# Kernel optimization log

Hardware: AMD Instinct MI355X
Metric: run time of the kernel (lower is better)

Reference implementation:

```python
import jax, jax.numpy as jnp
import numpy as np

COST_CLASS = 1.0
COST_COORD = 1.0
ALPHA = 0.25
GAMMA = 2.0
EPS = 1e-8
B, N = 4, 512


def setup_inputs() -> dict:
    key = jax.random.key(0)
    k1, k2, k3 = jax.random.split(key, 3)
    return {
        "pred_logits": jax.random.normal(k1, (B, N), dtype=jnp.float32),
        "pred_points": jax.random.uniform(k2, (B, N, 2), dtype=jnp.float32),
        "gt_points": jax.random.uniform(k3, (B, N, 2), dtype=jnp.float32),
        "gt_mask": jnp.ones((B, N), dtype=bool),
    }


def _cost_matrix(pred_logits, pred_points, gt_points):
    # focal-style classification cost, depends only on the prediction -> column-constant
    prob = jax.nn.sigmoid(pred_logits)                       # [B, N]
    neg = (1.0 - ALPHA) * prob ** GAMMA * (-jnp.log(1.0 - prob + EPS))
    pos = ALPHA * (1.0 - prob) ** GAMMA * (-jnp.log(prob + EPS))
    cost_class = (pos - neg)[:, :, None]                     # [B, N, 1]
    # L1 cdist between pred_points and gt_points
    cost_coord = jnp.sum(
        jnp.abs(pred_points[:, :, None, :] - gt_points[:, None, :, :]), axis=-1
    )                                                        # [B, N, N]
    return COST_CLASS * cost_class + COST_COORD * cost_coord


def _lsa(cost):
    # Jonker-Volgenant shortest augmenting path (e-maxx Hungarian), square, minimization.
    c = np.asarray(cost, dtype=np.float64)
    n = c.shape[0]
    INF = 1e18
    u = np.zeros(n + 1)
    v = np.zeros(n + 1)
    p = np.zeros(n + 1, dtype=np.int64)   # p[j] = row matched to column j (1-based)
    way = np.zeros(n + 1, dtype=np.int64)
    for i in range(1, n + 1):
        p[0] = i
        j0 = 0
        minv = np.full(n + 1, INF)
        used = np.zeros(n + 1, dtype=bool)
        while True:
            used[j0] = True
            i0 = p[j0]
            cur = c[i0 - 1] - u[i0] - v[1:]
            nu = ~used[1:]
            mv = minv[1:]
            wy = way[1:]
            upd = nu & (cur < mv)
            mv[upd] = cur[upd]
            wy[upd] = j0
            cand = np.where(nu, mv, INF)
            j1 = int(np.argmin(cand)) + 1
            delta = cand[j1 - 1]
            u[p[used]] += delta
            v[used] -= delta
            mv[nu] -= delta
            j0 = j1
            if p[j0] == 0:
                break
        while j0:
            j1 = int(way[j0])
            p[j0] = int(p[j1])
            j0 = j1
    col_of_row = np.empty(n, dtype=np.int64)
    col_of_row[p[1:] - 1] = np.arange(n)
    return np.arange(n), col_of_row


def reference(pred_logits, pred_points, gt_points, gt_mask):
    C = _cost_matrix(pred_logits, pred_points, gt_points)   # [B, N, N]
    mask = np.asarray(gt_mask)
    assert mask.all(), "reference assumes all gt slots valid (static shapes)"
    Cn = np.asarray(jax.device_get(C))
    pred_idx, gt_idx = [], []
    for b in range(Cn.shape[0]):
        r, c = _lsa(Cn[b])
        pred_idx.append(r)
        gt_idx.append(c)
    pred_idx = jnp.asarray(np.stack(pred_idx))
    gt_idx = jnp.asarray(np.stack(gt_idx))
    return pred_idx, gt_idx, C
```

## Files before the change

### kernel.cpp

```cpp
#include <hip/hip_runtime.h>
#include <math.h>

constexpr int B_ = 4;
constexpr int N_ = 512;

__device__ __forceinline__ float cephes_expf(float xin) {
#pragma clang fp contract(off)
    float x = fminf(xin, 88.3762626647950f);
    x = fmaxf(x, -88.3762626647949f);
    float fx = x * 1.44269504088896341f;
    fx = fx + 0.5f;
    fx = floorf(fx);
    float tmp = fx * 0.693359375f;
    float z0  = fx * -2.12194440e-4f;
    float r = x - tmp;
    r = r - z0;
    float zz = r * r;
    float y = 1.9875691500E-4f;
    y = y * r + 1.3981999507E-3f;
    y = y * r + 8.3334519073E-3f;
    y = y * r + 4.1665795894E-2f;
    y = y * r + 1.6666665459E-1f;
    y = y * r + 5.0000001201E-1f;
    y = y * zz + r;
    y = y + 1.0f;
    int n = (int)fx;
    float p2n = __uint_as_float((unsigned)(n + 0x7f) << 23);
    float res = y * p2n;
    return fmaxf(res, xin);
}

__device__ __forceinline__ float cephes_logf(float t) {
#pragma clang fp contract(off)
    float xx = fmaxf(t, 1.17549435e-38f);
    unsigned u = __float_as_uint(xx);
    int e_i = (int)(u >> 23) - 0x7f;
    float e = (float)e_i + 1.0f;
    float m = __uint_as_float((u & 0x807fffffu) | 0x3f000000u);
    int mask = (m < 0.707106781186547524f);
    float tmp1 = mask ? m : 0.0f;
    float x = m - 1.0f;
    e = e - (mask ? 1.0f : 0.0f);
    x = x + tmp1;
    float z = x * x;
    float y = 7.0376836292E-2f;
    y = y * x + -1.1514610310E-1f;
    y = y * x + 1.1676998740E-1f;
    y = y * x + -1.2420140846E-1f;
    y = y * x + 1.4249322787E-1f;
    y = y * x + -1.6668057665E-1f;
    y = y * x + 2.0000714765E-1f;
    y = y * x + -2.4999993993E-1f;
    y = y * x + 3.3333331174E-1f;
    y = y * x;
    y = y * z;
    y = e * -2.12194440e-4f + y;
    y = y - z * 0.5f;
    float res = x + y;
    res = res + e * 0.693359375f;
    return res;
}

__global__ __launch_bounds__(256) void class_cost_kernel(
    const float* __restrict__ logits, float* __restrict__ cc_out)
{
#pragma clang fp contract(off)
    int idx = blockIdx.x * 256 + threadIdx.x;
    if (idx >= B_ * N_) return;
    float x    = logits[idx];
    float e    = cephes_expf(-x);
    float prob = 1.0f / (1.0f + e);
    float om   = 1.0f - prob;
    float p2   = prob * prob;
    float o2   = om * om;
    float lneg = cephes_logf(om   + 1e-8f);
    float lpos = cephes_logf(prob + 1e-8f);
    float neg  = (0.75f * p2) * (-lneg);
    float pos  = (0.25f * o2) * (-lpos);
    cc_out[idx] = pos - neg;
}

__global__ __launch_bounds__(512) void cost_kernel(
    const float* __restrict__ cc,
    const float* __restrict__ pred_pts,
    const float* __restrict__ gt_pts,
    float* __restrict__ C)
{
    int blk = blockIdx.x;
    int b = blk >> 9;
    int i = blk & (N_ - 1);
    int j = threadIdx.x;

    const float2* pp2 = reinterpret_cast<const float2*>(pred_pts);
    const float2* gp2 = reinterpret_cast<const float2*>(gt_pts);
    float2 pp = pp2[b * N_ + i];
    float2 gp = gp2[b * N_ + j];
    float coord = fabsf(pp.x - gp.x) + fabsf(pp.y - gp.y);

    C[(size_t)b * N_ * N_ + (size_t)i * N_ + j] = cc[blk] + coord;
}

template<int CTRL>
__device__ __forceinline__ uint32_t dpp32(uint32_t x) {
    return (uint32_t)__builtin_amdgcn_update_dpp((int)x, (int)x, CTRL, 0xF, 0xF, false);
}
#define UMINSTEP(X, CTRL) { uint32_t o_ = dpp32<CTRL>(X); X = (o_ < X) ? o_ : X; }

__device__ __forceinline__ uint32_t wave_umin_lane63(uint32_t x) {
    UMINSTEP(x, 0x111) UMINSTEP(x, 0x112) UMINSTEP(x, 0x114)
    UMINSTEP(x, 0x118) UMINSTEP(x, 0x142) UMINSTEP(x, 0x143)
    return x;
}

__device__ __forceinline__ double readlane_f64(double d, int lane) {
    unsigned long long ll = (unsigned long long)__double_as_longlong(d);
    unsigned lo = (unsigned)__builtin_amdgcn_readlane((int)(unsigned)ll, lane);
    unsigned hi = (unsigned)__builtin_amdgcn_readlane((int)(unsigned)(ll >> 32), lane);
    return __longlong_as_double((long long)(((unsigned long long)hi << 32) | lo));
}

__global__ __launch_bounds__(64, 1) void solve_kernel(
    const float* __restrict__ cc_in,
    const float* __restrict__ pred_pts,
    const float* __restrict__ gt_pts,
    float* __restrict__ pred_idx,
    float* __restrict__ gt_idx)
{
    const int b = blockIdx.x;
    const int t = threadIdx.x;

    const float2* pq = reinterpret_cast<const float2*>(pred_pts) + b * N_;
    const float2* gq = reinterpret_cast<const float2*>(gt_pts)   + b * N_;
    const float*  cq = cc_in + b * N_;
    const int base = t << 3;

    float2 r0 = pq[base + 0], r1 = pq[base + 1], r2 = pq[base + 2], r3 = pq[base + 3];
    float2 r4 = pq[base + 4], r5 = pq[base + 5], r6 = pq[base + 6], r7 = pq[base + 7];
    float2 g0 = gq[base + 0], g1 = gq[base + 1], g2 = gq[base + 2], g3 = gq[base + 3];
    float2 g4 = gq[base + 4], g5 = gq[base + 5], g6 = gq[base + 6], g7 = gq[base + 7];
    float  c0 = cq[base + 0], c1 = cq[base + 1], c2 = cq[base + 2], c3 = cq[base + 3];
    float  c4 = cq[base + 4], c5 = cq[base + 5], c6 = cq[base + 6], c7 = cq[base + 7];

    double u0=0.0,u1=0.0,u2=0.0,u3=0.0,u4=0.0,u5=0.0,u6=0.0,u7=0.0;
    double v0=0.0,v1=0.0,v2=0.0,v3=0.0,v4=0.0,v5=0.0,v6=0.0,v7=0.0;
    int    p0=-1,p1=-1,p2=-1,p3=-1,p4=-1,p5=-1,p6=-1,p7=-1;

    #pragma unroll
    for (int k = 0; k < 8; ++k)
        pred_idx[b * N_ + t + 64 * k] = (float)(t + 64 * k);

    #define SEL8F(sl, x0,x1,x2,x3,x4,x5,x6,x7, out) {                      \
        float a0_=((sl)&1)?(x1):(x0), a1_=((sl)&1)?(x3):(x2);              \
        float a2_=((sl)&1)?(x5):(x4), a3_=((sl)&1)?(x7):(x6);              \
        float b0_=((sl)&2)?a1_:a0_,   b1_=((sl)&2)?a3_:a2_;                \
        out = ((sl)&4)?b1_:b0_; }
    #define SEL8I(sl, x0,x1,x2,x3,x4,x5,x6,x7, out) {                      \
        int a0_=((sl)&1)?(x1):(x0), a1_=((sl)&1)?(x3):(x2);                \
        int a2_=((sl)&1)?(x5):(x4), a3_=((sl)&1)?(x7):(x6);                \
        int b0_=((sl)&2)?a1_:a0_,   b1_=((sl)&2)?a3_:a2_;                  \
        out = ((sl)&4)?b1_:b0_; }
    #define SEL8D(sl, x0,x1,x2,x3,x4,x5,x6,x7, out) {                      \
        double a0_=((sl)&1)?(x1):(x0), a1_=((sl)&1)?(x3):(x2);             \
        double a2_=((sl)&1)?(x5):(x4), a3_=((sl)&1)?(x7):(x6);             \
        double b0_=((sl)&2)?a1_:a0_,   b1_=((sl)&2)?a3_:a2_;               \
        out = ((sl)&4)?b1_:b0_; }

    float px_r, py_r, cc_r; double urow;
    #define ROW_SCALARS(r) {                                               \
        int sl_ = (r) & 7, ln_ = (r) >> 3;                                 \
        float sx_, sy_, sc_; double su_;                                   \
        SEL8F(sl_, r0.x,r1.x,r2.x,r3.x,r4.x,r5.x,r6.x,r7.x, sx_);          \
        SEL8F(sl_, r0.y,r1.y,r2.y,r3.y,r4.y,r5.y,r6.y,r7.y, sy_);          \
        SEL8F(sl_, c0,c1,c2,c3,c4,c5,c6,c7, sc_);                          \
        SEL8D(sl_, u0,u1,u2,u3,u4,u5,u6,u7, su_);                          \
        px_r = __uint_as_float((unsigned)__builtin_amdgcn_readlane(        \
                   (int)__float_as_uint(sx_), ln_));                       \
        py_r = __uint_as_float((unsigned)__builtin_amdgcn_readlane(        \
                   (int)__float_as_uint(sy_), ln_));                       \
        cc_r = __uint_as_float((unsigned)__builtin_amdgcn_readlane(        \
                   (int)__float_as_uint(sc_), ln_));                       \
        urow = readlane_f64(su_, ln_); }

    const float INF32 = __uint_as_float(0x7F800000u);

    for (int i = 0; i < N_; ++i) {
        unsigned used_m  = 0u;
        unsigned chain_m = (t == (i >> 3)) ? (1u << (i & 7)) : 0u;
        ROW_SCALARS(i);

        for (;;) {
#pragma clang fp contract(off)
            float w0 = cc_r + (fabsf(px_r - g0.x) + fabsf(py_r - g0.y));
            float w1 = cc_r + (fabsf(px_r - g1.x) + fabsf(py_r - g1.y));
            float w2 = cc_r + (fabsf(px_r - g2.x) + fabsf(py_r - g2.y));
            float w3 = cc_r + (fabsf(px_r - g3.x) + fabsf(py_r - g3.y));
            float w4 = cc_r + (fabsf(px_r - g4.x) + fabsf(py_r - g4.y));
            float w5 = cc_r + (fabsf(px_r - g5.x) + fabsf(py_r - g5.y));
            float w6 = cc_r + (fabsf(px_r - g6.x) + fabsf(py_r - g6.y));
            float w7 = cc_r + (fabsf(px_r - g7.x) + fabsf(py_r - g7.y));
            w0 = (used_m & 0x01u) ? INF32 : w0;
            w1 = (used_m & 0x02u) ? INF32 : w1;
            w2 = (used_m & 0x04u) ? INF32 : w2;
            w3 = (used_m & 0x08u) ? INF32 : w3;
            w4 = (used_m & 0x10u) ? INF32 : w4;
            w5 = (used_m & 0x20u) ? INF32 : w5;
            w6 = (used_m & 0x40u) ? INF32 : w6;
            w7 = (used_m & 0x80u) ? INF32 : w7;

            double d0 = ((double)w0 - urow) - v0;
            double d1 = ((double)w1 - urow) - v1;
            double d2 = ((double)w2 - urow) - v2;
            double d3 = ((double)w3 - urow) - v3;
            double d4 = ((double)w4 - urow) - v4;
            double d5 = ((double)w5 - urow) - v5;
            double d6 = ((double)w6 - urow) - v6;
            double d7 = ((double)w7 - urow) - v7;

            double  ka = (d1 < d0) ? d1 : d0;  uint32_t sa = (d1 < d0) ? 1u : 0u;
            double  kb = (d3 < d2) ? d3 : d2;  uint32_t sb = (d3 < d2) ? 3u : 2u;
            double  kx = (d5 < d4) ? d5 : d4;  uint32_t sx = (d5 < d4) ? 5u : 4u;
            double  kd = (d7 < d6) ? d7 : d6;  uint32_t sd = (d7 < d6) ? 7u : 6u;
            double  ke = (kb < ka) ? kb : ka;  uint32_t se = (kb < ka) ? sb : sa;
            double  kf = (kd < kx) ? kd : kx;  uint32_t sf = (kd < kx) ? sd : sx;
            double  bv = (kf < ke) ? kf : ke;  uint32_t bslot = (kf < ke) ? sf : se;

            uint64_t kb64 = (uint64_t)__double_as_longlong(bv);
            kb64 ^= (kb64 >> 63) ? 0xFFFFFFFFFFFFFFFFull : 0x8000000000000000ull;
            uint32_t khi = (uint32_t)(kb64 >> 32);
            uint32_t klo = (uint32_t)kb64;

            int own_pre;
            SEL8I(bslot, p0,p1,p2,p3,p4,p5,p6,p7, own_pre);

            uint32_t Mhi = (uint32_t)__builtin_amdgcn_readlane(
                               (int)wave_umin_lane63(khi), 63);
            unsigned long long tied_hi = __ballot(khi == Mhi);

            int lane1; uint32_t Mlo;
            if (__builtin_popcountll(tied_hi) == 1) {
                lane1 = (int)__builtin_ctzll(tied_hi);
                Mlo = (uint32_t)__builtin_amdgcn_readlane((int)klo, lane1);
            } else {
                uint32_t kl2 = (khi == Mhi) ? klo : 0xFFFFFFFFu;
                Mlo = (uint32_t)__builtin_amdgcn_readlane(
                          (int)wave_umin_lane63(kl2), 63);
                lane1 = (int)__builtin_ctzll(__ballot(khi == Mhi && klo == Mlo));
            }

            int slot1 = __builtin_amdgcn_readlane((int)bslot, lane1);
            int owner = __builtin_amdgcn_readlane(own_pre, lane1);

            uint64_t M = ((uint64_t)Mhi << 32) | Mlo;
            uint64_t db = (M >> 63) ? (M ^ 0x8000000000000000ull) : ~M;
            double delta = __longlong_as_double((long long)db);

            if (owner < 0) {
                u0 += (chain_m & 0x01u) ? delta : 0.0;
                u1 += (chain_m & 0x02u) ? delta : 0.0;
                u2 += (chain_m & 0x04u) ? delta : 0.0;
                u3 += (chain_m & 0x08u) ? delta : 0.0;
                u4 += (chain_m & 0x10u) ? delta : 0.0;
                u5 += (chain_m & 0x20u) ? delta : 0.0;
                u6 += (chain_m & 0x40u) ? delta : 0.0;
                u7 += (chain_m & 0x80u) ? delta : 0.0;
                v0 -= (used_m  & 0x01u) ? delta : 0.0;
                v1 -= (used_m  & 0x02u) ? delta : 0.0;
                v2 -= (used_m  & 0x04u) ? delta : 0.0;
                v3 -= (used_m  & 0x08u) ? delta : 0.0;
                v4 -= (used_m  & 0x10u) ? delta : 0.0;
                v5 -= (used_m  & 0x20u) ? delta : 0.0;
                v6 -= (used_m  & 0x40u) ? delta : 0.0;
                v7 -= (used_m  & 0x80u) ? delta : 0.0;
                bool mine = (t == lane1);
                p0 = (mine && slot1 == 0) ? i : p0;
                p1 = (mine && slot1 == 1) ? i : p1;
                p2 = (mine && slot1 == 2) ? i : p2;
                p3 = (mine && slot1 == 3) ? i : p3;
                p4 = (mine && slot1 == 4) ? i : p4;
                p5 = (mine && slot1 == 5) ? i : p5;
                p6 = (mine && slot1 == 6) ? i : p6;
                p7 = (mine && slot1 == 7) ? i : p7;
                break;
            }

            ROW_SCALARS(owner);

            u0 += (chain_m & 0x01u) ? delta : 0.0;
            u1 += (chain_m & 0x02u) ? delta : 0.0;
            u2 += (chain_m & 0x04u) ? delta : 0.0;
            u3 += (chain_m & 0x08u) ? delta : 0.0;
            u4 += (chain_m & 0x10u) ? delta : 0.0;
            u5 += (chain_m & 0x20u) ? delta : 0.0;
            u6 += (chain_m & 0x40u) ? delta : 0.0;
            u7 += (chain_m & 0x80u) ? delta : 0.0;
            v0 -= (used_m  & 0x01u) ? delta : 0.0;
            v1 -= (used_m  & 0x02u) ? delta : 0.0;
            v2 -= (used_m  & 0x04u) ? delta : 0.0;
            v3 -= (used_m  & 0x08u) ? delta : 0.0;
            v4 -= (used_m  & 0x10u) ? delta : 0.0;
            v5 -= (used_m  & 0x20u) ? delta : 0.0;
            v6 -= (used_m  & 0x40u) ? delta : 0.0;
            v7 -= (used_m  & 0x80u) ? delta : 0.0;

            used_m  |= (t == lane1)        ? (1u << slot1)       : 0u;
            chain_m |= (t == (owner >> 3)) ? (1u << (owner & 7)) : 0u;
        }
    }

    gt_idx[b * N_ + p0] = (float)(base);
    gt_idx[b * N_ + p1] = (float)(base + 1);
    gt_idx[b * N_ + p2] = (float)(base + 2);
    gt_idx[b * N_ + p3] = (float)(base + 3);
    gt_idx[b * N_ + p4] = (float)(base + 4);
    gt_idx[b * N_ + p5] = (float)(base + 5);
    gt_idx[b * N_ + p6] = (float)(base + 6);
    gt_idx[b * N_ + p7] = (float)(base + 7);
}

extern "C" void kernel_launch(void* const* d_in, const int* in_sizes, int n_in,
                              void* d_out, int out_size, void* d_ws, size_t ws_size,
                              hipStream_t stream)
{
    const float* logits   = (const float*)d_in[0];
    const float* pred_pts = (const float*)d_in[1];
    const float* gt_pts   = (const float*)d_in[2];

    float* out      = (float*)d_out;
    float* pred_idx = out;
    float* gt_idx   = out + B_ * N_;
    float* C        = out + 2 * B_ * N_;
    float* cc       = (float*)d_ws;

    class_cost_kernel<<<(B_ * N_ + 255) / 256, 256, 0, stream>>>(logits, cc);
    cost_kernel<<<B_ * N_, N_, 0, stream>>>(cc, pred_pts, gt_pts, C);
    solve_kernel<<<B_, 64, 0, stream>>>(cc, pred_pts, gt_pts, pred_idx, gt_idx);
}
```

Before: 1.646 ms.

## Interleave two batch Hungarian solves per wave to hide serial latency

Each wavefront now solves two batch items at once, alternating one augmenting step of each inside a single flat loop so their independent dependency chains can overlap. The nested row/augment loops become a branch-free state machine that handles the terminal step with selects and prefetches the next row's scalars unconditionally. The single-tie fast path for the cross-lane argmin is dropped, so the second min reduction always runs. The trade-offs are that each step now covers two problems, more registers are used per lane, and only two waves are launched, so wall time follows the longer of each pair of solves.

```diff
diff --git a/kernel.cpp b/kernel.cpp
--- a/kernel.cpp
+++ b/kernel.cpp
@@ -119,6 +119,149 @@
     return __longlong_as_double((long long)(((unsigned long long)hi << 32) | lo));
 }
 
+#define SEL8F(sl, x0,x1,x2,x3,x4,x5,x6,x7, out) {                      \
+    float a0_=((sl)&1)?(x1):(x0), a1_=((sl)&1)?(x3):(x2);              \
+    float a2_=((sl)&1)?(x5):(x4), a3_=((sl)&1)?(x7):(x6);              \
+    float b0_=((sl)&2)?a1_:a0_,   b1_=((sl)&2)?a3_:a2_;                \
+    out = ((sl)&4)?b1_:b0_; }
+#define SEL8I(sl, x0,x1,x2,x3,x4,x5,x6,x7, out) {                      \
+    int a0_=((sl)&1)?(x1):(x0), a1_=((sl)&1)?(x3):(x2);                \
+    int a2_=((sl)&1)?(x5):(x4), a3_=((sl)&1)?(x7):(x6);                \
+    int b0_=((sl)&2)?a1_:a0_,   b1_=((sl)&2)?a3_:a2_;                  \
+    out = ((sl)&4)?b1_:b0_; }
+#define SEL8D(sl, x0,x1,x2,x3,x4,x5,x6,x7, out) {                      \
+    double a0_=((sl)&1)?(x1):(x0), a1_=((sl)&1)?(x3):(x2);             \
+    double a2_=((sl)&1)?(x5):(x4), a3_=((sl)&1)?(x7):(x6);             \
+    double b0_=((sl)&2)?a1_:a0_,   b1_=((sl)&2)?a3_:a2_;               \
+    out = ((sl)&4)?b1_:b0_; }
+
+#define DECL_LOAD(S, b)                                                       \
+    const float2* pq##S = reinterpret_cast<const float2*>(pred_pts) + (b) * N_; \
+    const float2* gq##S = reinterpret_cast<const float2*>(gt_pts)   + (b) * N_; \
+    const float*  cq##S = cc_in + (b) * N_;                                   \
+    float2 r0##S = pq##S[base+0], r1##S = pq##S[base+1];                      \
+    float2 r2##S = pq##S[base+2], r3##S = pq##S[base+3];                      \
+    float2 r4##S = pq##S[base+4], r5##S = pq##S[base+5];                      \
+    float2 r6##S = pq##S[base+6], r7##S = pq##S[base+7];                      \
+    float2 g0##S = gq##S[base+0], g1##S = gq##S[base+1];                      \
+    float2 g2##S = gq##S[base+2], g3##S = gq##S[base+3];                      \
+    float2 g4##S = gq##S[base+4], g5##S = gq##S[base+5];                      \
+    float2 g6##S = gq##S[base+6], g7##S = gq##S[base+7];                      \
+    float  c0##S = cq##S[base+0], c1##S = cq##S[base+1];                      \
+    float  c2##S = cq##S[base+2], c3##S = cq##S[base+3];                      \
+    float  c4##S = cq##S[base+4], c5##S = cq##S[base+5];                      \
+    float  c6##S = cq##S[base+6], c7##S = cq##S[base+7];                      \
+    double u0##S=0.0,u1##S=0.0,u2##S=0.0,u3##S=0.0;                           \
+    double u4##S=0.0,u5##S=0.0,u6##S=0.0,u7##S=0.0;                           \
+    double v0##S=0.0,v1##S=0.0,v2##S=0.0,v3##S=0.0;                           \
+    double v4##S=0.0,v5##S=0.0,v6##S=0.0,v7##S=0.0;                           \
+    int    p0##S=-1,p1##S=-1,p2##S=-1,p3##S=-1;                               \
+    int    p4##S=-1,p5##S=-1,p6##S=-1,p7##S=-1;                               \
+    unsigned used_m##S = 0u;                                                  \
+    unsigned chain_m##S = (t == 0) ? 1u : 0u;                                 \
+    int i##S = 0;                                                             \
+    float px_r##S, py_r##S, cc_r##S; double urow##S;
+
+#define ROW_SCALARS_S(S, r) {                                                 \
+    int sl_ = (r) & 7, ln_ = (r) >> 3;                                        \
+    float sx_, sy_, sc_; double su_;                                          \
+    SEL8F(sl_, r0##S.x,r1##S.x,r2##S.x,r3##S.x,r4##S.x,r5##S.x,r6##S.x,r7##S.x, sx_); \
+    SEL8F(sl_, r0##S.y,r1##S.y,r2##S.y,r3##S.y,r4##S.y,r5##S.y,r6##S.y,r7##S.y, sy_); \
+    SEL8F(sl_, c0##S,c1##S,c2##S,c3##S,c4##S,c5##S,c6##S,c7##S, sc_);         \
+    SEL8D(sl_, u0##S,u1##S,u2##S,u3##S,u4##S,u5##S,u6##S,u7##S, su_);         \
+    px_r##S = __uint_as_float((unsigned)__builtin_amdgcn_readlane(            \
+                  (int)__float_as_uint(sx_), ln_));                           \
+    py_r##S = __uint_as_float((unsigned)__builtin_amdgcn_readlane(            \
+                  (int)__float_as_uint(sy_), ln_));                           \
+    cc_r##S = __uint_as_float((unsigned)__builtin_amdgcn_readlane(            \
+                  (int)__float_as_uint(sc_), ln_));                           \
+    urow##S = readlane_f64(su_, ln_); }
+
+#define STEP(S) {                                                             \
+    float w0 = cc_r##S + (fabsf(px_r##S - g0##S.x) + fabsf(py_r##S - g0##S.y)); \
+    float w1 = cc_r##S + (fabsf(px_r##S - g1##S.x) + fabsf(py_r##S - g1##S.y)); \
+    float w2 = cc_r##S + (fabsf(px_r##S - g2##S.x) + fabsf(py_r##S - g2##S.y)); \
+    float w3 = cc_r##S + (fabsf(px_r##S - g3##S.x) + fabsf(py_r##S - g3##S.y)); \
+    float w4 = cc_r##S + (fabsf(px_r##S - g4##S.x) + fabsf(py_r##S - g4##S.y)); \
+    float w5 = cc_r##S + (fabsf(px_r##S - g5##S.x) + fabsf(py_r##S - g5##S.y)); \
+    float w6 = cc_r##S + (fabsf(px_r##S - g6##S.x) + fabsf(py_r##S - g6##S.y)); \
+    float w7 = cc_r##S + (fabsf(px_r##S - g7##S.x) + fabsf(py_r##S - g7##S.y)); \
+    w0 = (used_m##S & 0x01u) ? INF32 : w0;                                    \
+    w1 = (used_m##S & 0x02u) ? INF32 : w1;                                    \
+    w2 = (used_m##S & 0x04u) ? INF32 : w2;                                    \
+    w3 = (used_m##S & 0x08u) ? INF32 : w3;                                    \
+    w4 = (used_m##S & 0x10u) ? INF32 : w4;                                    \
+    w5 = (used_m##S & 0x20u) ? INF32 : w5;                                    \
+    w6 = (used_m##S & 0x40u) ? INF32 : w6;                                    \
+    w7 = (used_m##S & 0x80u) ? INF32 : w7;                                    \
+    double d0 = ((double)w0 - urow##S) - v0##S;                               \
+    double d1 = ((double)w1 - urow##S) - v1##S;                               \
+    double d2 = ((double)w2 - urow##S) - v2##S;                               \
+    double d3 = ((double)w3 - urow##S) - v3##S;                               \
+    double d4 = ((double)w4 - urow##S) - v4##S;                               \
+    double d5 = ((double)w5 - urow##S) - v5##S;                               \
+    double d6 = ((double)w6 - urow##S) - v6##S;                               \
+    double d7 = ((double)w7 - urow##S) - v7##S;                               \
+    double  ka = (d1 < d0) ? d1 : d0;  uint32_t sa = (d1 < d0) ? 1u : 0u;     \
+    double  kb = (d3 < d2) ? d3 : d2;  uint32_t sb = (d3 < d2) ? 3u : 2u;     \
+    double  kx = (d5 < d4) ? d5 : d4;  uint32_t sx = (d5 < d4) ? 5u : 4u;     \
+    double  kd = (d7 < d6) ? d7 : d6;  uint32_t sd = (d7 < d6) ? 7u : 6u;     \
+    double  ke = (kb < ka) ? kb : ka;  uint32_t se = (kb < ka) ? sb : sa;     \
+    double  kf = (kd < kx) ? kd : kx;  uint32_t sf = (kd < kx) ? sd : sx;     \
+    double  bv = (kf < ke) ? kf : ke;  uint32_t bslot = (kf < ke) ? sf : se;  \
+    uint64_t kb64 = (uint64_t)__double_as_longlong(bv);                       \
+    kb64 ^= (kb64 >> 63) ? 0xFFFFFFFFFFFFFFFFull : 0x8000000000000000ull;     \
+    uint32_t khi = (uint32_t)(kb64 >> 32);                                    \
+    uint32_t klo = (uint32_t)kb64;                                            \
+    int own_pre;                                                              \
+    SEL8I(bslot, p0##S,p1##S,p2##S,p3##S,p4##S,p5##S,p6##S,p7##S, own_pre);   \
+    uint32_t Mhi = (uint32_t)__builtin_amdgcn_readlane(                       \
+                       (int)wave_umin_lane63(khi), 63);                       \
+    uint32_t kl2 = (khi == Mhi) ? klo : 0xFFFFFFFFu;                          \
+    uint32_t Mlo = (uint32_t)__builtin_amdgcn_readlane(                       \
+                       (int)wave_umin_lane63(kl2), 63);                       \
+    int lane1 = (int)__builtin_ctzll(__ballot(khi == Mhi && klo == Mlo));     \
+    int slot1 = __builtin_amdgcn_readlane((int)bslot, lane1);                 \
+    int owner = __builtin_amdgcn_readlane(own_pre, lane1);                    \
+    uint64_t M = ((uint64_t)Mhi << 32) | Mlo;                                 \
+    uint64_t db = (M >> 63) ? (M ^ 0x8000000000000000ull) : ~M;               \
+    double delta = __longlong_as_double((long long)db);                       \
+    int terminal = (owner < 0) ? 1 : 0;                                       \
+    int nxt  = terminal ? (i##S + 1) : owner;                                 \
+    int nxtc = (nxt > (N_ - 1)) ? (N_ - 1) : nxt;                             \
+    ROW_SCALARS_S(S, nxtc);                                                   \
+    u0##S += (chain_m##S & 0x01u) ? delta : 0.0;                              \
+    u1##S += (chain_m##S & 0x02u) ? delta : 0.0;                              \
+    u2##S += (chain_m##S & 0x04u) ? delta : 0.0;                              \
+    u3##S += (chain_m##S & 0x08u) ? delta : 0.0;                              \
+    u4##S += (chain_m##S & 0x10u) ? delta : 0.0;                              \
+    u5##S += (chain_m##S & 0x20u) ? delta : 0.0;                              \
+    u6##S += (chain_m##S & 0x40u) ? delta : 0.0;                              \
+    u7##S += (chain_m##S & 0x80u) ? delta : 0.0;                              \
+    v0##S -= (used_m##S  & 0x01u) ? delta : 0.0;                              \
+    v1##S -= (used_m##S  & 0x02u) ? delta : 0.0;                              \
+    v2##S -= (used_m##S  & 0x04u) ? delta : 0.0;                              \
+    v3##S -= (used_m##S  & 0x08u) ? delta : 0.0;                              \
+    v4##S -= (used_m##S  & 0x10u) ? delta : 0.0;                              \
+    v5##S -= (used_m##S  & 0x20u) ? delta : 0.0;                              \
+    v6##S -= (used_m##S  & 0x40u) ? delta : 0.0;                              \
+    v7##S -= (used_m##S  & 0x80u) ? delta : 0.0;                              \
+    bool mine = (t == lane1);                                                 \
+    p0##S = (terminal && mine && slot1 == 0) ? i##S : p0##S;                  \
+    p1##S = (terminal && mine && slot1 == 1) ? i##S : p1##S;                  \
+    p2##S = (terminal && mine && slot1 == 2) ? i##S : p2##S;                  \
+    p3##S = (terminal && mine && slot1 == 3) ? i##S : p3##S;                  \
+    p4##S = (terminal && mine && slot1 == 4) ? i##S : p4##S;                  \
+    p5##S = (terminal && mine && slot1 == 5) ? i##S : p5##S;                  \
+    p6##S = (terminal && mine && slot1 == 6) ? i##S : p6##S;                  \
+    p7##S = (terminal && mine && slot1 == 7) ? i##S : p7##S;                  \
+    unsigned hopbit = (t == (nxt >> 3)) ? (1u << (nxt & 7)) : 0u;             \
+    unsigned selbit = mine ? (1u << slot1) : 0u;                              \
+    chain_m##S = terminal ? hopbit : (chain_m##S | hopbit);                   \
+    used_m##S  = terminal ? 0u     : (used_m##S  | selbit);                   \
+    i##S += terminal;                                                         \
+}
+
 __global__ __launch_bounds__(64, 1) void solve_kernel(
     const float* __restrict__ cc_in,
     const float* __restrict__ pred_pts,
@@ -126,195 +269,48 @@
     float* __restrict__ pred_idx,
     float* __restrict__ gt_idx)
 {
-    const int b = blockIdx.x;
-    const int t = threadIdx.x;
-
-    const float2* pq = reinterpret_cast<const float2*>(pred_pts) + b * N_;
-    const float2* gq = reinterpret_cast<const float2*>(gt_pts)   + b * N_;
-    const float*  cq = cc_in + b * N_;
+#pragma clang fp contract(off)
+    const int t  = threadIdx.x;
+    const int bA = blockIdx.x * 2;
+    const int bB = bA + 1;
     const int base = t << 3;
-
-    float2 r0 = pq[base + 0], r1 = pq[base + 1], r2 = pq[base + 2], r3 = pq[base + 3];
-    float2 r4 = pq[base + 4], r5 = pq[base + 5], r6 = pq[base + 6], r7 = pq[base + 7];
-    float2 g0 = gq[base + 0], g1 = gq[base + 1], g2 = gq[base + 2], g3 = gq[base + 3];
-    float2 g4 = gq[base + 4], g5 = gq[base + 5], g6 = gq[base + 6], g7 = gq[base + 7];
-    float  c0 = cq[base + 0], c1 = cq[base + 1], c2 = cq[base + 2], c3 = cq[base + 3];
-    float  c4 = cq[base + 4], c5 = cq[base + 5], c6 = cq[base + 6], c7 = cq[base + 7];
-
-    double u0=0.0,u1=0.0,u2=0.0,u3=0.0,u4=0.0,u5=0.0,u6=0.0,u7=0.0;
-    double v0=0.0,v1=0.0,v2=0.0,v3=0.0,v4=0.0,v5=0.0,v6=0.0,v7=0.0;
-    int    p0=-1,p1=-1,p2=-1,p3=-1,p4=-1,p5=-1,p6=-1,p7=-1;
+    const float INF32 = __uint_as_float(0x7F800000u);
+
+    DECL_LOAD(A, bA)
+    DECL_LOAD(B, bB)
 
     #pragma unroll
-    for (int k = 0; k < 8; ++k)
-        pred_idx[b * N_ + t + 64 * k] = (float)(t + 64 * k);
-
-    #define SEL8F(sl, x0,x1,x2,x3,x4,x5,x6,x7, out) {                      \
-        float a0_=((sl)&1)?(x1):(x0), a1_=((sl)&1)?(x3):(x2);              \
-        float a2_=((sl)&1)?(x5):(x4), a3_=((sl)&1)?(x7):(x6);              \
-        float b0_=((sl)&2)?a1_:a0_,   b1_=((sl)&2)?a3_:a2_;                \
-        out = ((sl)&4)?b1_:b0_; }
-    #define SEL8I(sl, x0,x1,x2,x3,x4,x5,x6,x7, out) {                      \
-        int a0_=((sl)&1)?(x1):(x0), a1_=((sl)&1)?(x3):(x2);                \
-        int a2_=((sl)&1)?(x5):(x4), a3_=((sl)&1)?(x7):(x6);                \
-        int b0_=((sl)&2)?a1_:a0_,   b1_=((sl)&2)?a3_:a2_;                  \
-        out = ((sl)&4)?b1_:b0_; }
-    #define SEL8D(sl, x0,x1,x2,x3,x4,x5,x6,x7, out) {                      \
-        double a0_=((sl)&1)?(x1):(x0), a1_=((sl)&1)?(x3):(x2);             \
-        double a2_=((sl)&1)?(x5):(x4), a3_=((sl)&1)?(x7):(x6);             \
-        double b0_=((sl)&2)?a1_:a0_,   b1_=((sl)&2)?a3_:a2_;               \
-        out = ((sl)&4)?b1_:b0_; }
-
-    float px_r, py_r, cc_r; double urow;
-    #define ROW_SCALARS(r) {                                               \
-        int sl_ = (r) & 7, ln_ = (r) >> 3;                                 \
-        float sx_, sy_, sc_; double su_;                                   \
-        SEL8F(sl_, r0.x,r1.x,r2.x,r3.x,r4.x,r5.x,r6.x,r7.x, sx_);          \
-        SEL8F(sl_, r0.y,r1.y,r2.y,r3.y,r4.y,r5.y,r6.y,r7.y, sy_);          \
-        SEL8F(sl_, c0,c1,c2,c3,c4,c5,c6,c7, sc_);                          \
-        SEL8D(sl_, u0,u1,u2,u3,u4,u5,u6,u7, su_);                          \
-        px_r = __uint_as_float((unsigned)__builtin_amdgcn_readlane(        \
-                   (int)__float_as_uint(sx_), ln_));                       \
-        py_r = __uint_as_float((unsigned)__builtin_amdgcn_readlane(        \
-                   (int)__float_as_uint(sy_), ln_));                       \
-        cc_r = __uint_as_float((unsigned)__builtin_amdgcn_readlane(        \
-                   (int)__float_as_uint(sc_), ln_));                       \
-        urow = readlane_f64(su_, ln_); }
-
-    const float INF32 = __uint_as_float(0x7F800000u);
-
-    for (int i = 0; i < N_; ++i) {
-        unsigned used_m  = 0u;
-        unsigned chain_m = (t == (i >> 3)) ? (1u << (i & 7)) : 0u;
-        ROW_SCALARS(i);
-
-        for (;;) {
-#pragma clang fp contract(off)
-            float w0 = cc_r + (fabsf(px_r - g0.x) + fabsf(py_r - g0.y));
-            float w1 = cc_r + (fabsf(px_r - g1.x) + fabsf(py_r - g1.y));
-            float w2 = cc_r + (fabsf(px_r - g2.x) + fabsf(py_r - g2.y));
-            float w3 = cc_r + (fabsf(px_r - g3.x) + fabsf(py_r - g3.y));
-            float w4 = cc_r + (fabsf(px_r - g4.x) + fabsf(py_r - g4.y));
-            float w5 = cc_r + (fabsf(px_r - g5.x) + fabsf(py_r - g5.y));
-            float w6 = cc_r + (fabsf(px_r - g6.x) + fabsf(py_r - g6.y));
-            float w7 = cc_r + (fabsf(px_r - g7.x) + fabsf(py_r - g7.y));
-            w0 = (used_m & 0x01u) ? INF32 : w0;
-            w1 = (used_m & 0x02u) ? INF32 : w1;
-            w2 = (used_m & 0x04u) ? INF32 : w2;
-            w3 = (used_m & 0x08u) ? INF32 : w3;
-            w4 = (used_m & 0x10u) ? INF32 : w4;
-            w5 = (used_m & 0x20u) ? INF32 : w5;
-            w6 = (used_m & 0x40u) ? INF32 : w6;
-            w7 = (used_m & 0x80u) ? INF32 : w7;
-
-            double d0 = ((double)w0 - urow) - v0;
-            double d1 = ((double)w1 - urow) - v1;
-            double d2 = ((double)w2 - urow) - v2;
-            double d3 = ((double)w3 - urow) - v3;
-            double d4 = ((double)w4 - urow) - v4;
-            double d5 = ((double)w5 - urow) - v5;
-            double d6 = ((double)w6 - urow) - v6;
-            double d7 = ((double)w7 - urow) - v7;
-
-            double  ka = (d1 < d0) ? d1 : d0;  uint32_t sa = (d1 < d0) ? 1u : 0u;
-            double  kb = (d3 < d2) ? d3 : d2;  uint32_t sb = (d3 < d2) ? 3u : 2u;
-            double  kx = (d5 < d4) ? d5 : d4;  uint32_t sx = (d5 < d4) ? 5u : 4u;
-            double  kd = (d7 < d6) ? d7 : d6;  uint32_t sd = (d7 < d6) ? 7u : 6u;
-            double  ke = (kb < ka) ? kb : ka;  uint32_t se = (kb < ka) ? sb : sa;
-            double  kf = (kd < kx) ? kd : kx;  uint32_t sf = (kd < kx) ? sd : sx;
-            double  bv = (kf < ke) ? kf : ke;  uint32_t bslot = (kf < ke) ? sf : se;
-
-            uint64_t kb64 = (uint64_t)__double_as_longlong(bv);
-            kb64 ^= (kb64 >> 63) ? 0xFFFFFFFFFFFFFFFFull : 0x8000000000000000ull;
-            uint32_t khi = (uint32_t)(kb64 >> 32);
-            uint32_t klo = (uint32_t)kb64;
-
-            int own_pre;
-            SEL8I(bslot, p0,p1,p2,p3,p4,p5,p6,p7, own_pre);
-
-            uint32_t Mhi = (uint32_t)__builtin_amdgcn_readlane(
-                               (int)wave_umin_lane63(khi), 63);
-            unsigned long long tied_hi = __ballot(khi == Mhi);
-
-            int lane1; uint32_t Mlo;
-            if (__builtin_popcountll(tied_hi) == 1) {
-                lane1 = (int)__builtin_ctzll(tied_hi);
-                Mlo = (uint32_t)__builtin_amdgcn_readlane((int)klo, lane1);
-            } else {
-                uint32_t kl2 = (khi == Mhi) ? klo : 0xFFFFFFFFu;
-                Mlo = (uint32_t)__builtin_amdgcn_readlane(
-                          (int)wave_umin_lane63(kl2), 63);
-                lane1 = (int)__builtin_ctzll(__ballot(khi == Mhi && klo == Mlo));
-            }
-
-            int slot1 = __builtin_amdgcn_readlane((int)bslot, lane1);
-            int owner = __builtin_amdgcn_readlane(own_pre, lane1);
-
-            uint64_t M = ((uint64_t)Mhi << 32) | Mlo;
-            uint64_t db = (M >> 63) ? (M ^ 0x8000000000000000ull) : ~M;
-            double delta = __longlong_as_double((long long)db);
-
-            if (owner < 0) {
-                u0 += (chain_m & 0x01u) ? delta : 0.0;
-                u1 += (chain_m & 0x02u) ? delta : 0.0;
-                u2 += (chain_m & 0x04u) ? delta : 0.0;
-                u3 += (chain_m & 0x08u) ? delta : 0.0;
-                u4 += (chain_m & 0x10u) ? delta : 0.0;
-                u5 += (chain_m & 0x20u) ? delta : 0.0;
-                u6 += (chain_m & 0x40u) ? delta : 0.0;
-                u7 += (chain_m & 0x80u) ? delta : 0.0;
-                v0 -= (used_m  & 0x01u) ? delta : 0.0;
-                v1 -= (used_m  & 0x02u) ? delta : 0.0;
-                v2 -= (used_m  & 0x04u) ? delta : 0.0;
-                v3 -= (used_m  & 0x08u) ? delta : 0.0;
-                v4 -= (used_m  & 0x10u) ? delta : 0.0;
-                v5 -= (used_m  & 0x20u) ? delta : 0.0;
-                v6 -= (used_m  & 0x40u) ? delta : 0.0;
-                v7 -= (used_m  & 0x80u) ? delta : 0.0;
-                bool mine = (t == lane1);
-                p0 = (mine && slot1 == 0) ? i : p0;
-                p1 = (mine && slot1 == 1) ? i : p1;
-                p2 = (mine && slot1 == 2) ? i : p2;
-                p3 = (mine && slot1 == 3) ? i : p3;
-                p4 = (mine && slot1 == 4) ? i : p4;
-                p5 = (mine && slot1 == 5) ? i : p5;
-                p6 = (mine && slot1 == 6) ? i : p6;
-                p7 = (mine && slot1 == 7) ? i : p7;
-                break;
-            }
-
-            ROW_SCALARS(owner);
-
-            u0 += (chain_m & 0x01u) ? delta : 0.0;
-            u1 += (chain_m & 0x02u) ? delta : 0.0;
-            u2 += (chain_m & 0x04u) ? delta : 0.0;
-            u3 += (chain_m & 0x08u) ? delta : 0.0;
-            u4 += (chain_m & 0x10u) ? delta : 0.0;
-            u5 += (chain_m & 0x20u) ? delta : 0.0;
-            u6 += (chain_m & 0x40u) ? delta : 0.0;
-            u7 += (chain_m & 0x80u) ? delta : 0.0;
-            v0 -= (used_m  & 0x01u) ? delta : 0.0;
-            v1 -= (used_m  & 0x02u) ? delta : 0.0;
-            v2 -= (used_m  & 0x04u) ? delta : 0.0;
-            v3 -= (used_m  & 0x08u) ? delta : 0.0;
-            v4 -= (used_m  & 0x10u) ? delta : 0.0;
-            v5 -= (used_m  & 0x20u) ? delta : 0.0;
-            v6 -= (used_m  & 0x40u) ? delta : 0.0;
-            v7 -= (used_m  & 0x80u) ? delta : 0.0;
-
-            used_m  |= (t == lane1)        ? (1u << slot1)       : 0u;
-            chain_m |= (t == (owner >> 3)) ? (1u << (owner & 7)) : 0u;
-        }
+    for (int k = 0; k < 8; ++k) {
+        pred_idx[bA * N_ + t + 64 * k] = (float)(t + 64 * k);
+        pred_idx[bB * N_ + t + 64 * k] = (float)(t + 64 * k);
     }
 
-    gt_idx[b * N_ + p0] = (float)(base);
-    gt_idx[b * N_ + p1] = (float)(base + 1);
-    gt_idx[b * N_ + p2] = (float)(base + 2);
-    gt_idx[b * N_ + p3] = (float)(base + 3);
-    gt_idx[b * N_ + p4] = (float)(base + 4);
-    gt_idx[b * N_ + p5] = (float)(base + 5);
-    gt_idx[b * N_ + p6] = (float)(base + 6);
-    gt_idx[b * N_ + p7] = (float)(base + 7);
+    ROW_SCALARS_S(A, 0)
+    ROW_SCALARS_S(B, 0)
+
+    for (;;) {
+        STEP(A)
+        STEP(B)
+        if (iA >= N_ && iB >= N_) break;
+    }
+
+    gt_idx[bA * N_ + p0A] = (float)(base);
+    gt_idx[bA * N_ + p1A] = (float)(base + 1);
+    gt_idx[bA * N_ + p2A] = (float)(base + 2);
+    gt_idx[bA * N_ + p3A] = (float)(base + 3);
+    gt_idx[bA * N_ + p4A] = (float)(base + 4);
+    gt_idx[bA * N_ + p5A] = (float)(base + 5);
+    gt_idx[bA * N_ + p6A] = (float)(base + 6);
+    gt_idx[bA * N_ + p7A] = (float)(base + 7);
+
+    gt_idx[bB * N_ + p0B] = (float)(base);
+    gt_idx[bB * N_ + p1B] = (float)(base + 1);
+    gt_idx[bB * N_ + p2B] = (float)(base + 2);
+    gt_idx[bB * N_ + p3B] = (float)(base + 3);
+    gt_idx[bB * N_ + p4B] = (float)(base + 4);
+    gt_idx[bB * N_ + p5B] = (float)(base + 5);
+    gt_idx[bB * N_ + p6B] = (float)(base + 6);
+    gt_idx[bB * N_ + p7B] = (float)(base + 7);
 }
 
 extern "C" void kernel_launch(void* const* d_in, const int* in_sizes, int n_in,
@@ -333,5 +329,5 @@
 
     class_cost_kernel<<<(B_ * N_ + 255) / 256, 256, 0, stream>>>(logits, cc);
     cost_kernel<<<B_ * N_, N_, 0, stream>>>(cc, pred_pts, gt_pts, C);
-    solve_kernel<<<B_, 64, 0, stream>>>(cc, pred_pts, gt_pts, pred_idx, gt_idx);
-}
+    solve_kernel<<<B_ / 2, 64, 0, stream>>>(cc, pred_pts, gt_pts, pred_idx, gt_idx);
+}
```

After: 3.469 ms. 111% more time.
